# Optimization experiments

Measured on AMD Instinct MI355X. Metric: run time of the kernel, lower is better.

Reference implementation:

```python
import jax, jax.numpy as jnp
import numpy as np

B, S, D_MODEL, D_K = 4, 4096, 1024, 64


def setup_inputs() -> dict:
    key = jax.random.key(0)
    ks = jax.random.split(key, 4)
    scale = 1.0 / np.sqrt(D_MODEL)
    x = jax.random.normal(ks[0], (B, S, D_MODEL), dtype=jnp.float32)
    Wq = jax.random.normal(ks[1], (D_MODEL, D_K), dtype=jnp.float32) * scale
    Wk = jax.random.normal(ks[2], (D_MODEL, D_K), dtype=jnp.float32) * scale
    Wv = jax.random.normal(ks[3], (D_MODEL, D_K), dtype=jnp.float32) * scale
    bq = jnp.zeros((D_K,), dtype=jnp.float32)
    bk = jnp.zeros((D_K,), dtype=jnp.float32)
    bv = jnp.zeros((D_K,), dtype=jnp.float32)
    # causal mask: 1 = keep, 0 = masked (matches docstring semantics)
    mask = jnp.broadcast_to(
        jnp.tril(jnp.ones((S, S), dtype=jnp.int32))[None], (B, S, S)
    )
    return {"x": x, "mask": mask, "Wq": Wq, "bq": bq, "Wk": Wk, "bk": bk, "Wv": Wv, "bv": bv}


def reference(x, mask, Wq, bq, Wk, bk, Wv, bv):
    # Q/K/V projections: (B, S, d_model) @ (d_model, d_k) -> (B, S, d_k)
    Q = jnp.einsum("bsd,dk->bsk", x, Wq) + bq
    K = jnp.einsum("bsd,dk->bsk", x, Wk) + bk
    V = jnp.einsum("bsd,dk->bsk", x, Wv) + bv
    # scaled dot-product scores: (B, S, S)
    scores = jnp.einsum("bqk,bsk->bqs", Q, K) / jnp.sqrt(jnp.float32(D_K))
    scores = jnp.where(mask == 0, jnp.float32(-jnp.inf), scores)
    attn = jax.nn.softmax(scores, axis=-1)
    # dropout with p_drop = 0.0 is identity
    out = jnp.einsum("bqs,bsk->bqk", attn, V)  # (B, S, d_k)
    return out
```

## Files before the change

### kernel.cpp

```cpp
#include <hip/hip_runtime.h>
#include <hip/hip_bf16.h>


typedef float  f32x4  __attribute__((ext_vector_type(4)));
typedef float  f32x16 __attribute__((ext_vector_type(16)));
typedef short  s16x8  __attribute__((ext_vector_type(8)));
typedef short  s16x4  __attribute__((ext_vector_type(4)));

#define MFMA16(A, B, C) __builtin_amdgcn_mfma_f32_16x16x32_bf16((A), (B), (C), 0, 0, 0)
#define MFMA32(A, B, C) __builtin_amdgcn_mfma_f32_32x32x16_bf16((A), (B), (C), 0, 0, 0)

static __device__ __forceinline__ ushort f2bf(float f) {
    union { float f; unsigned u; } v; v.f = f;
    unsigned u = v.u;
    unsigned r = (u + 0x7FFFu + ((u >> 16) & 1u)) >> 16;
    return (ushort)r;
}

static __device__ __forceinline__ f32x4 fzero() {
    f32x4 v; v[0] = v[1] = v[2] = v[3] = 0.f; return v;
}

__global__ __launch_bounds__(256) void prep_w(const float* __restrict__ Wq,
                                              const float* __restrict__ Wk,
                                              const float* __restrict__ Wv,
                                              short* __restrict__ Wt) {
    const int c = blockIdx.x;
    const int t = threadIdx.x;
    const float* src; int cc; float sc = 1.0f;
    if (c < 64)       { src = Wq; cc = c;       sc = 0.125f; }
    else if (c < 128) { src = Wk; cc = c - 64;  }
    else              { src = Wv; cc = c - 128; }
    const int k0 = t * 4;
    s16x4 o;
    #pragma unroll
    for (int i = 0; i < 4; ++i) o[i] = (short)f2bf(src[(size_t)(k0 + i) * 64 + cc] * sc);
    *(s16x4*)&Wt[(size_t)c * 1024 + k0] = o;
}

__global__ __launch_bounds__(256) void proj(const float* __restrict__ x,
                                            const short* __restrict__ Wt,
                                            const float* __restrict__ bq,
                                            const float* __restrict__ bk,
                                            const float* __restrict__ bv,
                                            short* __restrict__ Qb,
                                            short* __restrict__ Kb,
                                            short* __restrict__ Vt) {
    const int tid  = threadIdx.x;
    const int lane = tid & 63;
    const int w    = tid >> 6;
    const int m0   = blockIdx.x * 32;
    const int l15  = lane & 15, gr = lane >> 4;

    __shared__ short xs[2][32][136];

    const int srow = tid >> 3;
    const int sc8  = tid & 7;
    const float* sbase = x + (size_t)(m0 + srow) * 1024 + 4 * sc8;

    f32x4 acc[3][2];
    #pragma unroll
    for (int m = 0; m < 3; ++m)
        for (int n = 0; n < 2; ++n) acc[m][n] = fzero();

    const short* aptr = Wt + (size_t)(48 * w + l15) * 1024 + 8 * gr;

    f32x4 ld[4];
    #pragma unroll
    for (int i = 0; i < 4; ++i) ld[i] = *(const f32x4*)(sbase + 32 * i);
    #pragma unroll
    for (int i = 0; i < 4; ++i) {
        s16x4 o;
        #pragma unroll
        for (int j = 0; j < 4; ++j) o[j] = (short)f2bf(ld[i][j]);
        *(s16x4*)&xs[0][srow][4 * sc8 + 32 * i] = o;
    }
    __syncthreads();

    for (int c = 0; c < 8; ++c) {
        const int buf = c & 1;
        if (c < 7) {
            #pragma unroll
            for (int i = 0; i < 4; ++i) ld[i] = *(const f32x4*)(sbase + 128 * (c + 1) + 32 * i);
        }
        #pragma unroll
        for (int f = 0; f < 4; ++f) {
            const int ko = 128 * c + 32 * f;
            s16x8 a[3];
            #pragma unroll
            for (int m = 0; m < 3; ++m) a[m] = *(const s16x8*)(aptr + (size_t)m * 16 * 1024 + ko);
            s16x8 b[2];
            #pragma unroll
            for (int n = 0; n < 2; ++n) b[n] = *(const s16x8*)&xs[buf][16 * n + l15][32 * f + 8 * gr];
            #pragma unroll
            for (int m = 0; m < 3; ++m)
                for (int n = 0; n < 2; ++n) acc[m][n] = MFMA16(a[m], b[n], acc[m][n]);
        }
        if (c < 7) {
            #pragma unroll
            for (int i = 0; i < 4; ++i) {
                s16x4 o;
                #pragma unroll
                for (int j = 0; j < 4; ++j) o[j] = (short)f2bf(ld[i][j]);
                *(s16x4*)&xs[buf ^ 1][srow][4 * sc8 + 32 * i] = o;
            }
        }
        __syncthreads();
    }

    #pragma unroll
    for (int m = 0; m < 3; ++m) {
        const int c0 = 48 * w + 16 * m + 4 * gr;
        #pragma unroll
        for (int n = 0; n < 2; ++n) {
            const int row = m0 + 16 * n + l15;
            f32x4 v = acc[m][n];
            if (c0 < 64) {
                s16x4 o;
                #pragma unroll
                for (int r = 0; r < 4; ++r) o[r] = (short)f2bf(v[r] + 0.125f * bq[c0 + r]);
                *(s16x4*)&Qb[(size_t)row * 64 + c0] = o;
            } else if (c0 < 128) {
                s16x4 o;
                #pragma unroll
                for (int r = 0; r < 4; ++r) o[r] = (short)f2bf(v[r] + bk[c0 - 64 + r]);
                *(s16x4*)&Kb[(size_t)row * 64 + (c0 - 64)] = o;
            } else {
                const int b = row >> 12, s = row & 4095;
                #pragma unroll
                for (int r = 0; r < 4; ++r)
                    Vt[((size_t)b * 64 + (c0 - 128 + r)) * 4096 + s] =
                        (short)f2bf(v[r] + bv[c0 - 128 + r]);
            }
        }
    }
}

__global__ __launch_bounds__(256, 2) void attn(const short* __restrict__ Qb,
                                               const short* __restrict__ Kb,
                                               const short* __restrict__ Vt,
                                               float* __restrict__ out) {
    const int bid   = blockIdx.x;
    const int wgid  = (bid & 7) * 64 + (bid >> 3);
    const int batch = wgid >> 7;
    const int g     = 127 - (wgid & 127);
    const int q0    = g * 32;
    const int tid   = threadIdx.x, lane = tid & 63, w = tid >> 6;
    const int l31   = lane & 31, h = lane >> 5, kb = 4 * h;

    __shared__ float Om[4][32][68];
    __shared__ float Mm[4][32], Lm[4][32];

    const size_t row0 = (size_t)batch * 4096;

    const short* Qp = Qb + (row0 + q0 + l31) * 64 + 8 * h;
    s16x8 qf[4];
    #pragma unroll
    for (int kk = 0; kk < 4; ++kk) qf[kk] = *(const s16x8*)(Qp + 16 * kk);

    f32x16 oT0, oT1;
    #pragma unroll
    for (int r = 0; r < 16; ++r) { oT0[r] = 0.f; oT1[r] = 0.f; }
    float m = -1e30f, l_ = 0.f;

    const int nt = g + 1;
    const int t0 = (nt * w) >> 2, t1 = (nt * (w + 1)) >> 2;

    const short* Kp = Kb + (row0 + l31) * 64 + 8 * h;
    const short* Vp = Vt + ((size_t)batch * 64 + l31) * 4096 + 8 * h;

    for (int t = t0; t < t1; ++t) {
        const int j0 = t * 32;
        s16x8 kf[4], va[2][2];
        #pragma unroll
        for (int kk = 0; kk < 4; ++kk)
            kf[kk] = *(const s16x8*)(Kp + (size_t)j0 * 64 + 16 * kk);
        #pragma unroll
        for (int dt = 0; dt < 2; ++dt)
            #pragma unroll
            for (int kk = 0; kk < 2; ++kk)
                va[dt][kk] = *(const s16x8*)(Vp + (size_t)dt * 32 * 4096 + j0 + 16 * kk);

        f32x16 sacc;
        #pragma unroll
        for (int r = 0; r < 16; ++r) sacc[r] = 0.f;
        #pragma unroll
        for (int kk = 0; kk < 4; ++kk) sacc = MFMA32(kf[kk], qf[kk], sacc);

        if (j0 == q0) {
            #pragma unroll
            for (int r = 0; r < 16; ++r) {
                const int kvloc = (r & 3) + 8 * (r >> 2) + kb;
                if (kvloc > l31) sacc[r] = -1e30f;
            }
        }

        float sm = sacc[0];
        #pragma unroll
        for (int r = 1; r < 16; ++r) sm = fmaxf(sm, sacc[r]);
        sm = fmaxf(sm, __shfl_xor(sm, 32));
        const float mn = fmaxf(m, sm);
        const float sc = __expf(m - mn);
        m = mn;

        float p[16]; float ls = 0.f;
        #pragma unroll
        for (int r = 0; r < 16; ++r) { p[r] = __expf(sacc[r] - mn); ls += p[r]; }
        l_ = l_ * sc + ls + __shfl_xor(ls, 32);
        #pragma unroll
        for (int r = 0; r < 16; ++r) { oT0[r] *= sc; oT1[r] *= sc; }

        unsigned pw[8];
        #pragma unroll
        for (int i = 0; i < 8; ++i)
            asm("v_cvt_pk_bf16_f32 %0, %1, %2" : "=v"(pw[i]) : "v"(p[2 * i]), "v"(p[2 * i + 1]));
        asm volatile("v_permlane32_swap_b32 %0, %1" : "+v"(pw[0]), "+v"(pw[2]));
        asm volatile("v_permlane32_swap_b32 %0, %1" : "+v"(pw[1]), "+v"(pw[3]));
        asm volatile("v_permlane32_swap_b32 %0, %1" : "+v"(pw[4]), "+v"(pw[6]));
        asm volatile("v_permlane32_swap_b32 %0, %1" : "+v"(pw[5]), "+v"(pw[7]));
        union { unsigned u[4]; s16x8 v; } f0, f1;
        f0.u[0] = pw[0]; f0.u[1] = pw[1]; f0.u[2] = pw[2]; f0.u[3] = pw[3];
        f1.u[0] = pw[4]; f1.u[1] = pw[5]; f1.u[2] = pw[6]; f1.u[3] = pw[7];

        oT0 = MFMA32(va[0][0], f0.v, oT0);
        oT0 = MFMA32(va[0][1], f1.v, oT0);
        oT1 = MFMA32(va[1][0], f0.v, oT1);
        oT1 = MFMA32(va[1][1], f1.v, oT1);
    }

    #pragma unroll
    for (int rg = 0; rg < 4; ++rg) {
        f32x4 v0, v1;
        #pragma unroll
        for (int j = 0; j < 4; ++j) { v0[j] = oT0[4 * rg + j]; v1[j] = oT1[4 * rg + j]; }
        const int d0 = rg * 8 + kb;
        *(f32x4*)&Om[w][l31][d0]      = v0;
        *(f32x4*)&Om[w][l31][32 + d0] = v1;
    }
    if (lane < 32) { Mm[w][l31] = m; Lm[w][l31] = l_; }
    __syncthreads();

    {
        const int q = tid >> 3, d0 = (tid & 7) * 8;
        const float m0 = Mm[0][q], m1 = Mm[1][q], m2 = Mm[2][q], m3 = Mm[3][q];
        const float mt = fmaxf(fmaxf(m0, m1), fmaxf(m2, m3));
        float sw[4];
        sw[0] = __expf(m0 - mt); sw[1] = __expf(m1 - mt);
        sw[2] = __expf(m2 - mt); sw[3] = __expf(m3 - mt);
        const float lt = sw[0] * Lm[0][q] + sw[1] * Lm[1][q] + sw[2] * Lm[2][q] + sw[3] * Lm[3][q];
        const float inv = 1.f / lt;
        f32x4 a0 = fzero(), a1 = fzero();
        #pragma unroll
        for (int ww = 0; ww < 4; ++ww) {
            f32x4 u0 = *(const f32x4*)&Om[ww][q][d0];
            f32x4 u1 = *(const f32x4*)&Om[ww][q][d0 + 4];
            #pragma unroll
            for (int j = 0; j < 4; ++j) { a0[j] += sw[ww] * u0[j]; a1[j] += sw[ww] * u1[j]; }
        }
        const size_t ob = (row0 + q0 + q) * 64 + d0;
        f32x4 r0, r1;
        #pragma unroll
        for (int j = 0; j < 4; ++j) { r0[j] = a0[j] * inv; r1[j] = a1[j] * inv; }
        *(f32x4*)&out[ob]     = r0;
        *(f32x4*)&out[ob + 4] = r1;
    }
}

extern "C" void kernel_launch(void* const* d_in, const int* in_sizes, int n_in,
                              void* d_out, int out_size, void* d_ws, size_t ws_size,
                              hipStream_t stream) {
    const float* x  = (const float*)d_in[0];
    const float* Wq = (const float*)d_in[2];
    const float* bq = (const float*)d_in[3];
    const float* Wk = (const float*)d_in[4];
    const float* bk = (const float*)d_in[5];
    const float* Wv = (const float*)d_in[6];
    const float* bv = (const float*)d_in[7];
    float* out = (float*)d_out;

    char* ws = (char*)d_ws;
    short* Wt = (short*)(ws);
    short* Qb = (short*)(ws + 393216);
    short* Kb = (short*)(ws + 2490368);
    short* Vt = (short*)(ws + 4587520);

    prep_w<<<dim3(192), dim3(256), 0, stream>>>(Wq, Wk, Wv, Wt);
    proj<<<dim3(512), dim3(256), 0, stream>>>(x, Wt, bq, bk, bv, Qb, Kb, Vt);
    attn<<<dim3(512), dim3(256), 0, stream>>>(Qb, Kb, Vt, out);
}
```

Before: 94.09 us.

## Prefetch K/V and weight fragments, lazy softmax rescale, tiled weight transpose

Several changes land at once. The weight prep kernel now transposes through shared memory with coalesced vector loads and launches 48 blocks instead of 192. The projection kernel register double-buffers the weight fragments and pads its shared tile. The attention kernel prefetches the next K/V tile into registers, remaps blocks so each XCD serves one batch, uses tree reductions, and skips the online-softmax rescale unless the running max grows by more than 8. These target memory latency and ALU work, at the cost of extra register pressure and reliance on a bounded unnormalized exponent.

```diff
diff --git a/kernel.cpp b/kernel.cpp
--- a/kernel.cpp
+++ b/kernel.cpp
@@ -25,17 +25,30 @@
                                               const float* __restrict__ Wk,
                                               const float* __restrict__ Wv,
                                               short* __restrict__ Wt) {
-    const int c = blockIdx.x;
+    const int blk = blockIdx.x;
+    const int mat = blk >> 4, kt = blk & 15;
+    const float* src = mat == 0 ? Wq : (mat == 1 ? Wk : Wv);
+    const float sc = (mat == 0) ? 0.125f : 1.0f;
+    __shared__ float wsm[64][68];
     const int t = threadIdx.x;
-    const float* src; int cc; float sc = 1.0f;
-    if (c < 64)       { src = Wq; cc = c;       sc = 0.125f; }
-    else if (c < 128) { src = Wk; cc = c - 64;  }
-    else              { src = Wv; cc = c - 128; }
-    const int k0 = t * 4;
-    s16x4 o;
-    #pragma unroll
-    for (int i = 0; i < 4; ++i) o[i] = (short)f2bf(src[(size_t)(k0 + i) * 64 + cc] * sc);
-    *(s16x4*)&Wt[(size_t)c * 1024 + k0] = o;
+
+    const int rb = t >> 4, c4 = (t & 15) * 4;
+    #pragma unroll
+    for (int i = 0; i < 4; ++i) {
+        f32x4 v = *(const f32x4*)&src[(size_t)(kt * 64 + rb + 16 * i) * 64 + c4];
+        *(f32x4*)&wsm[rb + 16 * i][c4] = v;
+    }
+    __syncthreads();
+
+    const int c = t >> 2, ks = (t & 3) * 16;
+    s16x8 o0, o1;
+    #pragma unroll
+    for (int j = 0; j < 8; ++j) o0[j] = (short)f2bf(wsm[ks + j][c] * sc);
+    #pragma unroll
+    for (int j = 0; j < 8; ++j) o1[j] = (short)f2bf(wsm[ks + 8 + j][c] * sc);
+    const size_t ob = (size_t)(mat * 64 + c) * 1024 + kt * 64 + ks;
+    *(s16x8*)&Wt[ob]     = o0;
+    *(s16x8*)&Wt[ob + 8] = o1;
 }
 
 __global__ __launch_bounds__(256) void proj(const float* __restrict__ x,
@@ -52,7 +65,7 @@
     const int m0   = blockIdx.x * 32;
     const int l15  = lane & 15, gr = lane >> 4;
 
-    __shared__ short xs[2][32][136];
+    __shared__ short xs[2][32][140];
 
     const int srow = tid >> 3;
     const int sc8  = tid & 7;
@@ -75,6 +88,10 @@
         for (int j = 0; j < 4; ++j) o[j] = (short)f2bf(ld[i][j]);
         *(s16x4*)&xs[0][srow][4 * sc8 + 32 * i] = o;
     }
+
+    s16x8 a_cur[3], a_nxt[3];
+    #pragma unroll
+    for (int m = 0; m < 3; ++m) a_cur[m] = *(const s16x8*)(aptr + (size_t)m * 16 * 1024);
     __syncthreads();
 
     for (int c = 0; c < 8; ++c) {
@@ -86,15 +103,17 @@
         #pragma unroll
         for (int f = 0; f < 4; ++f) {
             const int ko = 128 * c + 32 * f;
-            s16x8 a[3];
-            #pragma unroll
-            for (int m = 0; m < 3; ++m) a[m] = *(const s16x8*)(aptr + (size_t)m * 16 * 1024 + ko);
+            const int kn = (ko + 32) & 1023;
+            #pragma unroll
+            for (int m = 0; m < 3; ++m) a_nxt[m] = *(const s16x8*)(aptr + (size_t)m * 16 * 1024 + kn);
             s16x8 b[2];
             #pragma unroll
             for (int n = 0; n < 2; ++n) b[n] = *(const s16x8*)&xs[buf][16 * n + l15][32 * f + 8 * gr];
             #pragma unroll
             for (int m = 0; m < 3; ++m)
-                for (int n = 0; n < 2; ++n) acc[m][n] = MFMA16(a[m], b[n], acc[m][n]);
+                for (int n = 0; n < 2; ++n) acc[m][n] = MFMA16(a_cur[m], b[n], acc[m][n]);
+            #pragma unroll
+            for (int m = 0; m < 3; ++m) a_cur[m] = a_nxt[m];
         }
         if (c < 7) {
             #pragma unroll
@@ -141,9 +160,9 @@
                                                const short* __restrict__ Vt,
                                                float* __restrict__ out) {
     const int bid   = blockIdx.x;
-    const int wgid  = (bid & 7) * 64 + (bid >> 3);
-    const int batch = wgid >> 7;
-    const int g     = 127 - (wgid & 127);
+    const int xcd   = bid & 7, bi = bid >> 3;
+    const int batch = xcd >> 1;
+    const int g     = 127 - 2 * bi - (xcd & 1);
     const int q0    = g * 32;
     const int tid   = threadIdx.x, lane = tid & 63, w = tid >> 6;
     const int l31   = lane & 31, h = lane >> 5, kb = 4 * h;
@@ -169,17 +188,30 @@
     const short* Kp = Kb + (row0 + l31) * 64 + 8 * h;
     const short* Vp = Vt + ((size_t)batch * 64 + l31) * 4096 + 8 * h;
 
+    s16x8 kf[4], va[2][2], kf2[4], va2[2][2];
+    if (t0 < t1) {
+        const int j0 = t0 * 32;
+        #pragma unroll
+        for (int kk = 0; kk < 4; ++kk) kf[kk] = *(const s16x8*)(Kp + (size_t)j0 * 64 + 16 * kk);
+        #pragma unroll
+        for (int dt = 0; dt < 2; ++dt)
+            #pragma unroll
+            for (int kk = 0; kk < 2; ++kk)
+                va[dt][kk] = *(const s16x8*)(Vp + (size_t)dt * 32 * 4096 + j0 + 16 * kk);
+    }
+
     for (int t = t0; t < t1; ++t) {
         const int j0 = t * 32;
-        s16x8 kf[4], va[2][2];
-        #pragma unroll
-        for (int kk = 0; kk < 4; ++kk)
-            kf[kk] = *(const s16x8*)(Kp + (size_t)j0 * 64 + 16 * kk);
-        #pragma unroll
-        for (int dt = 0; dt < 2; ++dt)
-            #pragma unroll
-            for (int kk = 0; kk < 2; ++kk)
-                va[dt][kk] = *(const s16x8*)(Vp + (size_t)dt * 32 * 4096 + j0 + 16 * kk);
+        if (t + 1 < t1) {
+            const int jn = j0 + 32;
+            #pragma unroll
+            for (int kk = 0; kk < 4; ++kk) kf2[kk] = *(const s16x8*)(Kp + (size_t)jn * 64 + 16 * kk);
+            #pragma unroll
+            for (int dt = 0; dt < 2; ++dt)
+                #pragma unroll
+                for (int kk = 0; kk < 2; ++kk)
+                    va2[dt][kk] = *(const s16x8*)(Vp + (size_t)dt * 32 * 4096 + jn + 16 * kk);
+        }
 
         f32x16 sacc;
         #pragma unroll
@@ -195,20 +227,33 @@
             }
         }
 
-        float sm = sacc[0];
-        #pragma unroll
-        for (int r = 1; r < 16; ++r) sm = fmaxf(sm, sacc[r]);
-        sm = fmaxf(sm, __shfl_xor(sm, 32));
-        const float mn = fmaxf(m, sm);
-        const float sc = __expf(m - mn);
-        m = mn;
-
-        float p[16]; float ls = 0.f;
-        #pragma unroll
-        for (int r = 0; r < 16; ++r) { p[r] = __expf(sacc[r] - mn); ls += p[r]; }
-        l_ = l_ * sc + ls + __shfl_xor(ls, 32);
-        #pragma unroll
-        for (int r = 0; r < 16; ++r) { oT0[r] *= sc; oT1[r] *= sc; }
+        float tm[8];
+        #pragma unroll
+        for (int r = 0; r < 8; ++r) tm[r] = fmaxf(sacc[r], sacc[r + 8]);
+        #pragma unroll
+        for (int r = 0; r < 4; ++r) tm[r] = fmaxf(tm[r], tm[r + 4]);
+        tm[0] = fmaxf(fmaxf(tm[0], tm[2]), fmaxf(tm[1], tm[3]));
+        float sm = fmaxf(tm[0], __shfl_xor(tm[0], 32));
+
+        if (!__all(sm - m <= 8.f)) {
+            const float mn = fmaxf(m, sm);
+            const float sc = __expf(m - mn);
+            m = mn;
+            l_ *= sc;
+            #pragma unroll
+            for (int r = 0; r < 16; ++r) { oT0[r] *= sc; oT1[r] *= sc; }
+        }
+
+        float p[16];
+        #pragma unroll
+        for (int r = 0; r < 16; ++r) p[r] = __expf(sacc[r] - m);
+        float ts[8];
+        #pragma unroll
+        for (int r = 0; r < 8; ++r) ts[r] = p[r] + p[r + 8];
+        #pragma unroll
+        for (int r = 0; r < 4; ++r) ts[r] = ts[r] + ts[r + 4];
+        const float ls = (ts[0] + ts[2]) + (ts[1] + ts[3]);
+        l_ += ls + __shfl_xor(ls, 32);
 
         unsigned pw[8];
         #pragma unroll
@@ -226,6 +271,13 @@
         oT0 = MFMA32(va[0][1], f1.v, oT0);
         oT1 = MFMA32(va[1][0], f0.v, oT1);
         oT1 = MFMA32(va[1][1], f1.v, oT1);
+
+        #pragma unroll
+        for (int kk = 0; kk < 4; ++kk) kf[kk] = kf2[kk];
+        #pragma unroll
+        for (int dt = 0; dt < 2; ++dt)
+            #pragma unroll
+            for (int kk = 0; kk < 2; ++kk) va[dt][kk] = va2[dt][kk];
     }
 
     #pragma unroll
@@ -284,7 +336,7 @@
     short* Kb = (short*)(ws + 2490368);
     short* Vt = (short*)(ws + 4587520);
 
-    prep_w<<<dim3(192), dim3(256), 0, stream>>>(Wq, Wk, Wv, Wt);
+    prep_w<<<dim3(48), dim3(256), 0, stream>>>(Wq, Wk, Wv, Wt);
     proj<<<dim3(512), dim3(256), 0, stream>>>(x, Wt, bq, bk, bv, Qb, Kb, Vt);
     attn<<<dim3(512), dim3(256), 0, stream>>>(Qb, Kb, Vt, out);
 }
```

New measurement: 85.31 us. 1.1x faster.
